# Kernel tuning notes

Hardware: AMD Instinct MI355X
Metric: run time of the kernel (lower is better)

The kernel has to match this reference:

```python
import jax, jax.numpy as jnp
import numpy as np

DIM = 1280
HEADS = 16
HEAD_DIM = DIM // HEADS  # 80
N_CHUNKS = 8
CHUNK = 1024
TOTAL = N_CHUNKS * CHUNK  # 8192 packed tokens


def rotate_half(x):
    x1, x2 = jnp.split(x, 2, axis=-1)
    return jnp.concatenate([-x2, x1], axis=-1)


def setup_inputs() -> dict:
    key = jax.random.key(0)
    k0, k1, k2 = jax.random.split(key, 3)
    hidden_states = jax.random.normal(k0, (TOTAL, DIM), dtype=jnp.float32)
    # 2D-rope style per-token angles, duplicated halves (standard vision RoPE layout)
    inv_freq = 1.0 / (10000.0 ** (jnp.arange(0, HEAD_DIM, 2, dtype=jnp.float32) / HEAD_DIM))
    pos = jnp.arange(TOTAL, dtype=jnp.float32)
    freqs = pos[:, None] * inv_freq[None, :]            # [T, HEAD_DIM//2]
    emb = jnp.concatenate([freqs, freqs], axis=-1)      # [T, HEAD_DIM]
    cos = jnp.cos(emb)
    sin = jnp.sin(emb)
    qkv_w = jax.random.normal(k1, (3 * DIM, DIM), dtype=jnp.float32) * 0.02
    qkv_b = jnp.zeros((3 * DIM,), dtype=jnp.float32)
    proj_w = jax.random.normal(k2, (DIM, DIM), dtype=jnp.float32) * 0.02
    proj_b = jnp.zeros((DIM,), dtype=jnp.float32)
    cu_seqlens = (jnp.arange(N_CHUNKS + 1, dtype=jnp.int32) * CHUNK)
    return {"hidden_states": hidden_states, "cos": cos, "sin": sin,
            "qkv_w": qkv_w, "qkv_b": qkv_b, "proj_w": proj_w, "proj_b": proj_b,
            "cu_seqlens": cu_seqlens}


def reference(hidden_states, cos, sin, qkv_w, qkv_b, proj_w, proj_b, cu_seqlens):
    # Equal-length chunks (cu_seqlens uniform): vectorize the Python chunk loop
    # as a leading batch axis n over chunks of length L.
    n = cu_seqlens.shape[0] - 1
    total, dim = hidden_states.shape
    L = total // n
    scaling = HEAD_DIM ** -0.5

    x = hidden_states.reshape(n, L, dim)
    qkv = x @ qkv_w.T + qkv_b                              # [n, L, 3*dim]
    qkv = qkv.reshape(n, L, 3, HEADS, HEAD_DIM)
    q, k, v = qkv[:, :, 0], qkv[:, :, 1], qkv[:, :, 2]     # [n, L, H, hd]

    # inline RoPE in fp32 (matches apply_rotary_pos_emb_vision)
    c = cos.reshape(n, L, 1, HEAD_DIM).astype(jnp.float32)
    s = sin.reshape(n, L, 1, HEAD_DIM).astype(jnp.float32)
    qf = q.astype(jnp.float32)
    kf = k.astype(jnp.float32)
    q = (qf * c + rotate_half(qf) * s).astype(q.dtype)
    k = (kf * c + rotate_half(kf) * s).astype(k.dtype)

    # naive per-chunk full attention: QK^T, fp32 softmax, PV
    scores = jnp.einsum('nlhd,nmhd->nhlm', q, k) * scaling  # [n, H, L, L]
    probs = jax.nn.softmax(scores.astype(jnp.float32), axis=-1).astype(q.dtype)
    out = jnp.einsum('nhlm,nmhd->nlhd', probs, v)           # [n, L, H, hd]
    out = out.reshape(n, L, dim)
    out = out @ proj_w.T + proj_b                           # [n, L, dim]
    return out.reshape(total, dim)
```

## Files before the change

kernel.cpp:

```cpp
#include <hip/hip_runtime.h>
#include <stdint.h>

#define DIM 1280
#define HEADS 16
#define HD 80
#define TOTAL 8192
#define CHUNK 1024
#define QKVN 3840

typedef __attribute__((ext_vector_type(8))) __bf16 bf16x8;
typedef __attribute__((ext_vector_type(4))) float floatx4;

typedef __attribute__((address_space(1))) const uint32_t gu32;
typedef __attribute__((address_space(3))) uint32_t lu32;

__device__ __forceinline__ void llds16(const void* g, void* l) {
  __builtin_amdgcn_global_load_lds((gu32*)g, (lu32*)l, 16, 0, 0);
}

__device__ __forceinline__ unsigned short f2b(float f) {
  union { __bf16 b; unsigned short u; } x; x.b = (__bf16)f; return x.u;
}
__device__ __forceinline__ float b2f(unsigned short u) {
  union { __bf16 b; unsigned short u; } x; x.u = u; return (float)x.b;
}
__device__ __forceinline__ float fexp2(float x) {
#if __has_builtin(__builtin_amdgcn_exp2f)
  return __builtin_amdgcn_exp2f(x);
#else
  return __expf(x * 0.6931471805599453f);
#endif
}

#define QSCALE (0.11180339887498949f * 1.44269504088896340f)

#define QROW 96
#define KT_SH (64 * 104)
#define VT_SH (80 * 72)

__global__ void cvt_bf16(const float* __restrict__ src, unsigned short* __restrict__ dst, int n4) {
  int i = blockIdx.x * 256 + threadIdx.x;
  if (i >= n4) return;
  float4 v = reinterpret_cast<const float4*>(src)[i];
  ushort4 o;
  o.x = f2b(v.x); o.y = f2b(v.y); o.z = f2b(v.z); o.w = f2b(v.w);
  reinterpret_cast<ushort4*>(dst)[i] = o;
}


__device__ __forceinline__ void stage_a64(const unsigned short* __restrict__ G,
                                          unsigned short* ls, int wv, int lane,
                                          int row0, int kk, int hi) {
#pragma unroll
  for (int t = 0; t < 2; ++t) {
    const int stripe = t * 8 + wv;
    const int rb = ((stripe >> 3) << 7) + ((stripe & 7) << 3) + hi;
    const int r = rb + (lane >> 3);
    const int ch = (lane & 7) ^ (r & 7);
    llds16(G + (size_t)(row0 + r) * DIM + kk + (ch << 3), ls + rb * 64);
  }
}

__device__ __forceinline__ void stage_b64(const unsigned short* __restrict__ G,
                                          unsigned short* ls, int wv, int lane,
                                          int row0, int kk, int hi) {
#pragma unroll
  for (int t = 0; t < 2; ++t) {
    const int stripe = t * 8 + wv;
    const int rb = ((stripe >> 2) << 6) + ((stripe & 3) << 3) + hi;
    const int r = rb + (lane >> 3);
    const int ch = (lane & 7) ^ (r & 7);
    llds16(G + (size_t)(row0 + r) * DIM + kk + (ch << 3), ls + rb * 64);
  }
}

__device__ __forceinline__ bf16x8 frg(const unsigned short* ls, int r, int cx) {
  return *reinterpret_cast<const bf16x8*>(ls + r * 64 + (cx << 3));
}

#define MFMA_BF16 __builtin_amdgcn_mfma_f32_16x16x32_bf16
#define LGKM0() asm volatile("s_waitcnt lgkmcnt(0)" ::: "memory")
#define BARR()  asm volatile("s_barrier" ::: "memory")

template<int MODE>
__launch_bounds__(512, 2)
__global__ void gemm8(const unsigned short* __restrict__ A,
                      const unsigned short* __restrict__ B,
                      const float* __restrict__ bias,
                      unsigned short* __restrict__ qo,
                      unsigned short* __restrict__ ko,
                      unsigned short* __restrict__ vo,
                      float* __restrict__ fo) {
  __shared__ __attribute__((aligned(16))) unsigned short lsA[2][256 * 64];
  __shared__ __attribute__((aligned(16))) unsigned short lsB[2][256 * 64];
  const int m0 = blockIdx.x * 256;
  const int n0 = blockIdx.y * 256;
  const int tid = threadIdx.x;
  const int wv = tid >> 6, lane = tid & 63;
  const int wr = wv >> 2, wc = wv & 3;
  const int q4 = lane >> 4, l15 = lane & 15;
  const int sx = l15 & 7;
  const int cx0 = q4 ^ sx;
  const int cx1 = (4 + q4) ^ sx;

  stage_a64(A, &lsA[0][0], wv, lane, m0, 0, 0);
  stage_b64(B, &lsB[0][0], wv, lane, n0, 0, 0);
  stage_b64(B, &lsB[0][0], wv, lane, n0, 0, 32);
  stage_a64(A, &lsA[0][0], wv, lane, m0, 0, 64);
  stage_b64(B, &lsB[1][0], wv, lane, n0, 64, 0);
  stage_a64(A, &lsA[1][0], wv, lane, m0, 64, 0);
  stage_b64(B, &lsB[1][0], wv, lane, n0, 64, 32);

  floatx4 acc[8][4];
#pragma unroll
  for (int i = 0; i < 8; ++i)
#pragma unroll
    for (int j = 0; j < 4; ++j)
      acc[i][j] = (floatx4){0.f, 0.f, 0.f, 0.f};

  asm volatile("s_waitcnt vmcnt(6)" ::: "memory");
  BARR();

  const int rA = wr * 128 + l15;
  const int rB = wc * 64 + l15;

  bf16x8 ArLo[4][2], ArHi[4][2], Blo[2][2], Bhi[2][2];

#pragma unroll 2
  for (int kt = 0; kt < 20; ++kt) {
    const unsigned short* la = &lsA[kt & 1][0];
    const unsigned short* lb = &lsB[kt & 1][0];
    unsigned short* aN = &lsA[(kt & 1) ^ 1][0];
    unsigned short* aC = &lsA[kt & 1][0];
    unsigned short* bC = &lsB[kt & 1][0];
    const bool st1 = (kt + 1 < 20);
    const bool st2 = (kt + 2 < 20);

    if (kt > 0) {
#pragma unroll
      for (int m = 0; m < 4; ++m)
#pragma unroll
        for (int n = 0; n < 2; ++n) {
          acc[m + 4][n] = MFMA_BF16(ArHi[m][0], Blo[n][0], acc[m + 4][n], 0, 0, 0);
          acc[m + 4][n] = MFMA_BF16(ArHi[m][1], Blo[n][1], acc[m + 4][n], 0, 0, 0);
        }
    }
#pragma unroll
    for (int m = 0; m < 4; ++m) {
      ArLo[m][0] = frg(la, rA + m * 16, cx0);
      ArLo[m][1] = frg(la, rA + m * 16, cx1);
    }
#pragma unroll
    for (int n = 0; n < 2; ++n) {
      Blo[n][0] = frg(lb, rB + n * 16, cx0);
      Blo[n][1] = frg(lb, rB + n * 16, cx1);
    }
    if (st1) stage_a64(A, aN, wv, lane, m0, (kt + 1) * 64, 64);
    LGKM0();
    BARR();

#pragma unroll
    for (int m = 0; m < 4; ++m)
#pragma unroll
      for (int n = 0; n < 2; ++n) {
        acc[m][n] = MFMA_BF16(ArLo[m][0], Blo[n][0], acc[m][n], 0, 0, 0);
        acc[m][n] = MFMA_BF16(ArLo[m][1], Blo[n][1], acc[m][n], 0, 0, 0);
      }
#pragma unroll
    for (int n = 0; n < 2; ++n) {
      Bhi[n][0] = frg(lb, rB + (n + 2) * 16, cx0);
      Bhi[n][1] = frg(lb, rB + (n + 2) * 16, cx1);
    }
    if (st2) stage_b64(B, bC, wv, lane, n0, (kt + 2) * 64, 0);
    LGKM0();
    BARR();

#pragma unroll
    for (int m = 0; m < 4; ++m)
#pragma unroll
      for (int n = 0; n < 2; ++n) {
        acc[m][n + 2] = MFMA_BF16(ArLo[m][0], Bhi[n][0], acc[m][n + 2], 0, 0, 0);
        acc[m][n + 2] = MFMA_BF16(ArLo[m][1], Bhi[n][1], acc[m][n + 2], 0, 0, 0);
      }
#pragma unroll
    for (int m = 0; m < 4; ++m) {
      ArHi[m][0] = frg(la, rA + (m + 4) * 16, cx0);
      ArHi[m][1] = frg(la, rA + (m + 4) * 16, cx1);
    }
    if (st2) stage_a64(A, aC, wv, lane, m0, (kt + 2) * 64, 0);
    LGKM0();
    BARR();

#pragma unroll
    for (int m = 0; m < 4; ++m)
#pragma unroll
      for (int n = 0; n < 2; ++n) {
        acc[m + 4][n + 2] = MFMA_BF16(ArHi[m][0], Bhi[n][0], acc[m + 4][n + 2], 0, 0, 0);
        acc[m + 4][n + 2] = MFMA_BF16(ArHi[m][1], Bhi[n][1], acc[m + 4][n + 2], 0, 0, 0);
      }
    if (st2) stage_b64(B, bC, wv, lane, n0, (kt + 2) * 64, 32);
    if (st2)      asm volatile("s_waitcnt vmcnt(6)" ::: "memory");
    else if (st1) asm volatile("s_waitcnt vmcnt(0)" ::: "memory");
    BARR();
  }

#pragma unroll
  for (int m = 0; m < 4; ++m)
#pragma unroll
    for (int n = 0; n < 2; ++n) {
      acc[m + 4][n] = MFMA_BF16(ArHi[m][0], Blo[n][0], acc[m + 4][n], 0, 0, 0);
      acc[m + 4][n] = MFMA_BF16(ArHi[m][1], Blo[n][1], acc[m + 4][n], 0, 0, 0);
    }

  if (MODE == 0) {
    if (blockIdx.y >= 10) {
      unsigned short* scr = (wv < 4) ? (&lsA[0][0] + wv * 8192)
                                     : (&lsB[0][0] + (wv - 4) * 8192);
      const int base_c = n0 - 2 * DIM + wc * 64;
#pragma unroll
      for (int n = 0; n < 4; ++n) {
        const int cloc = n * 16 + l15;
        const float bn = bias[2 * DIM + base_c + cloc];
        const int swz = (cloc & 7) << 4;
#pragma unroll
        for (int m = 0; m < 8; ++m) {
          const int rloc = m * 16 + q4 * 4;
          ushort4 w;
          w.x = f2b(acc[m][n][0] + bn);
          w.y = f2b(acc[m][n][1] + bn);
          w.z = f2b(acc[m][n][2] + bn);
          w.w = f2b(acc[m][n][3] + bn);
          *reinterpret_cast<ushort4*>(scr + cloc * 128 + (rloc ^ swz)) = w;
        }
      }
#pragma unroll
      for (int jtc = 0; jtc < 2; ++jtc) {
        const int rowg = m0 + wr * 128 + jtc * 64;
        const int chn = rowg >> 10, jtn = (rowg >> 6) & 15;
#pragma unroll
        for (int cb = 0; cb < 16; ++cb) {
          const int col = cb * 4 + q4;
          const int c = base_c + col;
          const int h = c / 80;
          const int d = c - h * 80;
          const int rloc = jtc * 64 + l15 * 4;
          const ushort4 w = *reinterpret_cast<const ushort4*>(
              scr + col * 128 + (rloc ^ ((col & 7) << 4)));
          *reinterpret_cast<ushort4*>(
              vo + (size_t)((chn * 16 + h) * 16 + jtn) * VT_SH + d * 72 + l15 * 4) = w;
        }
      }
      return;
    }
    unsigned short* os;
    int nloc = n0;
    if (blockIdx.y < 5) { os = qo; }
    else                { os = ko; nloc = n0 - DIM; }
#pragma unroll
    for (int n = 0; n < 4; ++n) {
      const int cg = wc * 64 + n * 16 + l15;
      const float bn = bias[n0 + cg];
#pragma unroll
      for (int m = 0; m < 8; ++m) {
#pragma unroll
        for (int r = 0; r < 4; ++r) {
          const int row = m0 + wr * 128 + m * 16 + q4 * 4 + r;
          os[(size_t)row * DIM + nloc + cg] = f2b(acc[m][n][r] + bn);
        }
      }
    }
    return;
  }
#pragma unroll
  for (int n = 0; n < 4; ++n) {
    const int cg = wc * 64 + n * 16 + l15;
    const float bn = bias[n0 + cg];
#pragma unroll
    for (int m = 0; m < 8; ++m) {
#pragma unroll
      for (int r = 0; r < 4; ++r) {
        const int row = m0 + wr * 128 + m * 16 + q4 * 4 + r;
        fo[(size_t)row * DIM + n0 + cg] = acc[m][n][r] + bn;
      }
    }
  }
}

__global__ void prep_qk(const unsigned short* __restrict__ qbuf,
                        const unsigned short* __restrict__ kbuf,
                        const float* __restrict__ cp, const float* __restrict__ sp,
                        unsigned short* __restrict__ qimg,
                        unsigned short* __restrict__ kimg) {
  const int m = blockIdx.x, tid = threadIdx.x;
  const int ch = m >> 10, rl = m & 1023;
  const int jt = rl >> 6, rr = rl & 63;

  if (tid < 160) {
    const int h = tid / 10, j = tid - h * 10;
    const int d0 = 4 * j;
    const float4 c4 = *reinterpret_cast<const float4*>(cp + (size_t)m * HD + d0);
    const float4 s4 = *reinterpret_cast<const float4*>(sp + (size_t)m * HD + d0);
    {
      const ushort4 lo = *reinterpret_cast<const ushort4*>(qbuf + (size_t)m * DIM + h * HD + d0);
      const ushort4 hi = *reinterpret_cast<const ushort4*>(qbuf + (size_t)m * DIM + h * HD + d0 + 40);
      ushort4 o1, o2;
      o1.x = f2b((b2f(lo.x) * c4.x - b2f(hi.x) * s4.x) * QSCALE);
      o1.y = f2b((b2f(lo.y) * c4.y - b2f(hi.y) * s4.y) * QSCALE);
      o1.z = f2b((b2f(lo.z) * c4.z - b2f(hi.z) * s4.z) * QSCALE);
      o1.w = f2b((b2f(lo.w) * c4.w - b2f(hi.w) * s4.w) * QSCALE);
      o2.x = f2b((b2f(hi.x) * c4.x + b2f(lo.x) * s4.x) * QSCALE);
      o2.y = f2b((b2f(hi.y) * c4.y + b2f(lo.y) * s4.y) * QSCALE);
      o2.z = f2b((b2f(hi.z) * c4.z + b2f(lo.z) * s4.z) * QSCALE);
      o2.w = f2b((b2f(hi.w) * c4.w + b2f(lo.w) * s4.w) * QSCALE);
      const size_t ob = ((size_t)(ch * 16 + h) * 1024 + rl) * QROW;
      *reinterpret_cast<ushort4*>(qimg + ob + d0) = o1;
      *reinterpret_cast<ushort4*>(qimg + ob + d0 + 40) = o2;
    }
    {
      const ushort4 lo = *reinterpret_cast<const ushort4*>(kbuf + (size_t)m * DIM + h * HD + d0);
      const ushort4 hi = *reinterpret_cast<const ushort4*>(kbuf + (size_t)m * DIM + h * HD + d0 + 40);
      ushort4 o1, o2;
      o1.x = f2b(b2f(lo.x) * c4.x - b2f(hi.x) * s4.x);
      o1.y = f2b(b2f(lo.y) * c4.y - b2f(hi.y) * s4.y);
      o1.z = f2b(b2f(lo.z) * c4.z - b2f(hi.z) * s4.z);
      o1.w = f2b(b2f(lo.w) * c4.w - b2f(hi.w) * s4.w);
      o2.x = f2b(b2f(hi.x) * c4.x + b2f(lo.x) * s4.x);
      o2.y = f2b(b2f(hi.y) * c4.y + b2f(lo.y) * s4.y);
      o2.z = f2b(b2f(hi.z) * c4.z + b2f(lo.z) * s4.z);
      o2.w = f2b(b2f(hi.w) * c4.w + b2f(lo.w) * s4.w);
      const size_t ob = ((size_t)((ch * 16 + h) * 16 + jt) * KT_SH) + rr * 104;
      *reinterpret_cast<ushort4*>(kimg + ob + d0) = o1;
      *reinterpret_cast<ushort4*>(kimg + ob + d0 + 40) = o2;
    }
  }
  if (tid < 64) {
    const int h = tid >> 2, qi = tid & 3;
    const size_t ob = ((size_t)(ch * 16 + h) * 1024 + rl) * QROW;
    *reinterpret_cast<ushort4*>(qimg + ob + 80 + 4 * qi) = (ushort4){0, 0, 0, 0};
  } else if (tid < 160) {
    const int t = tid - 64;
    const int h = t / 6, qi = t - h * 6;
    const size_t ob = ((size_t)((ch * 16 + h) * 16 + jt) * KT_SH) + rr * 104;
    *reinterpret_cast<ushort4*>(kimg + ob + 80 + 4 * qi) = (ushort4){0, 0, 0, 0};
  }
}

__launch_bounds__(256, 2)
__global__ void attn_k(const unsigned short* __restrict__ qimg,
                       const unsigned short* __restrict__ kimg,
                       const unsigned short* __restrict__ vimg,
                       unsigned short* __restrict__ ob) {
  __shared__ __attribute__((aligned(16))) unsigned short lsK[2][KT_SH];
  __shared__ __attribute__((aligned(16))) unsigned short lsV[2][VT_SH];
  __shared__ __attribute__((aligned(16))) unsigned short lsP[128 * 72];

  const int bx = blockIdx.x;
  const int qt = bx & 7, h = (bx >> 3) & 15, ch = bx >> 7;
  const int tid = threadIdx.x, wv = tid >> 6, lane = tid & 63;
  const int q4 = lane >> 4, l15 = lane & 15;
  const int qrow_loc = qt * 128 + wv * 32;

  bf16x8 aq[2][3];
  {
    const unsigned short* qb = qimg + ((size_t)(ch * 16 + h) * 1024 + qrow_loc) * QROW;
#pragma unroll
    for (int mt = 0; mt < 2; ++mt)
#pragma unroll
      for (int ks = 0; ks < 3; ++ks)
        aq[mt][ks] = *reinterpret_cast<const bf16x8*>(qb + (size_t)(mt * 16 + l15) * QROW + ks * 32 + q4 * 8);
  }

  floatx4 oacc[2][5];
  float lpart[2] = {0.f, 0.f};
#pragma unroll
  for (int mt = 0; mt < 2; ++mt)
#pragma unroll
    for (int t = 0; t < 5; ++t) oacc[mt][t] = (floatx4){0.f, 0.f, 0.f, 0.f};

  const char* kbase = (const char*)(kimg + (size_t)(ch * 16 + h) * 16 * KT_SH);
  const char* vbase = (const char*)(vimg + (size_t)(ch * 16 + h) * 16 * VT_SH);

  auto stage_kv = [&](int jt, char* lk, char* lv) {
    const char* kg = kbase + (size_t)jt * (KT_SH * 2);
#pragma unroll
    for (int r = 0; r < 4; ++r) {
      const int off = (r * 4 + wv) * 1024;
      if (off < KT_SH * 2)
        llds16(kg + off + lane * 16, lk + off);
    }
    const char* vg = vbase + (size_t)jt * (VT_SH * 2);
#pragma unroll
    for (int r = 0; r < 3; ++r) {
      const int off = (r * 4 + wv) * 1024;
      if (off < VT_SH * 2) {
        if (off + 1024 <= VT_SH * 2) llds16(vg + off + lane * 16, lv + off);
        else if (lane < 16)          llds16(vg + off + lane * 16, lv + off);
      }
    }
  };

  stage_kv(0, (char*)lsK[0], (char*)lsV[0]);

  for (int jt = 0; jt < 16; ++jt) {
    const int cur = jt & 1;
    __syncthreads();
    if (jt + 1 < 16)
      stage_kv(jt + 1, (char*)lsK[cur ^ 1], (char*)lsV[cur ^ 1]);

    const unsigned short* lk = lsK[cur];
    const unsigned short* lv = lsV[cur];

    floatx4 sfr[2][4];
    __builtin_amdgcn_s_setprio(1);
#pragma unroll
    for (int c = 0; c < 4; ++c) {
      const bf16x8 ak0 = *reinterpret_cast<const bf16x8*>(&lk[(c * 16 + l15) * 104 + 0  + q4 * 8]);
      const bf16x8 ak1 = *reinterpret_cast<const bf16x8*>(&lk[(c * 16 + l15) * 104 + 32 + q4 * 8]);
      const bf16x8 ak2 = *reinterpret_cast<const bf16x8*>(&lk[(c * 16 + l15) * 104 + 64 + q4 * 8]);
#pragma unroll
      for (int mt = 0; mt < 2; ++mt) {
        floatx4 s = (floatx4){0.f, 0.f, 0.f, 0.f};
        s = __builtin_amdgcn_mfma_f32_16x16x32_bf16(ak0, aq[mt][0], s, 0, 0, 0);
        s = __builtin_amdgcn_mfma_f32_16x16x32_bf16(ak1, aq[mt][1], s, 0, 0, 0);
        s = __builtin_amdgcn_mfma_f32_16x16x32_bf16(ak2, aq[mt][2], s, 0, 0, 0);
        sfr[mt][c] = s;
      }
    }
    __builtin_amdgcn_s_setprio(0);

#pragma unroll
    for (int mt = 0; mt < 2; ++mt)
#pragma unroll
      for (int c = 0; c < 4; ++c) {
        const float p0 = fexp2(sfr[mt][c][0]);
        const float p1 = fexp2(sfr[mt][c][1]);
        const float p2 = fexp2(sfr[mt][c][2]);
        const float p3 = fexp2(sfr[mt][c][3]);
        lpart[mt] += (p0 + p1) + (p2 + p3);
        ushort4 w;
        w.x = f2b(p0); w.y = f2b(p1); w.z = f2b(p2); w.w = f2b(p3);
        *reinterpret_cast<ushort4*>(&lsP[(wv * 32 + mt * 16 + l15) * 72 + c * 16 + q4 * 4]) = w;
      }

    __builtin_amdgcn_s_setprio(1);
#pragma unroll
    for (int ks = 0; ks < 2; ++ks) {
      const bf16x8 ap0 = *reinterpret_cast<const bf16x8*>(&lsP[(wv * 32 + 0  + l15) * 72 + ks * 32 + q4 * 8]);
      const bf16x8 ap1 = *reinterpret_cast<const bf16x8*>(&lsP[(wv * 32 + 16 + l15) * 72 + ks * 32 + q4 * 8]);
#pragma unroll
      for (int t = 0; t < 5; ++t) {
        const bf16x8 bv = *reinterpret_cast<const bf16x8*>(&lv[(t * 16 + l15) * 72 + ks * 32 + q4 * 8]);
        oacc[0][t] = __builtin_amdgcn_mfma_f32_16x16x32_bf16(ap0, bv, oacc[0][t], 0, 0, 0);
        oacc[1][t] = __builtin_amdgcn_mfma_f32_16x16x32_bf16(ap1, bv, oacc[1][t], 0, 0, 0);
      }
    }
    __builtin_amdgcn_s_setprio(0);
  }

#pragma unroll
  for (int mt = 0; mt < 2; ++mt) {
    lpart[mt] += __shfl_xor(lpart[mt], 16, 64);
    lpart[mt] += __shfl_xor(lpart[mt], 32, 64);
  }
  float inv[2];
  inv[0] = 1.0f / lpart[0];
  inv[1] = 1.0f / lpart[1];

  float invr[2][4];
#pragma unroll
  for (int mt = 0; mt < 2; ++mt)
#pragma unroll
    for (int r = 0; r < 4; ++r)
      invr[mt][r] = __shfl(inv[mt], q4 * 4 + r, 64);

#pragma unroll
  for (int mt = 0; mt < 2; ++mt)
#pragma unroll
    for (int t = 0; t < 5; ++t)
#pragma unroll
      for (int r = 0; r < 4; ++r) {
        const int gr = ch * CHUNK + qrow_loc + mt * 16 + q4 * 4 + r;
        const int gc = h * HD + t * 16 + l15;
        ob[(size_t)gr * DIM + gc] = f2b(oacc[mt][t][r] * invr[mt][r]);
      }
}

extern "C" void kernel_launch(void* const* d_in, const int* in_sizes, int n_in,
                              void* d_out, int out_size, void* d_ws, size_t ws_size,
                              hipStream_t stream) {
  (void)in_sizes; (void)n_in; (void)out_size; (void)ws_size;
  const float* hs    = (const float*)d_in[0];
  const float* cosp  = (const float*)d_in[1];
  const float* sinp  = (const float*)d_in[2];
  const float* qkvw  = (const float*)d_in[3];
  const float* qkvb  = (const float*)d_in[4];
  const float* projw = (const float*)d_in[5];
  const float* projb = (const float*)d_in[6];

  char* ws = (char*)d_ws;
  unsigned short* xb   = (unsigned short*)(ws + 0);
  unsigned short* wq   = (unsigned short*)(ws + 20971520);
  unsigned short* qbuf = (unsigned short*)(ws + 30801920);
  unsigned short* kbuf = (unsigned short*)(ws + 51773440);
  unsigned short* vimg = (unsigned short*)(ws + 72744960);
  unsigned short* wp   = (unsigned short*)(ws + 96337920);
  unsigned short* kimg = (unsigned short*)(ws + 99614720);
  unsigned short* qimg = (unsigned short*)(ws + 0);
  unsigned short* obuf = qbuf;

  cvt_bf16<<<TOTAL * DIM / 4 / 256, 256, 0, stream>>>(hs, xb, TOTAL * DIM / 4);
  cvt_bf16<<<QKVN * DIM / 4 / 256, 256, 0, stream>>>(qkvw, wq, QKVN * DIM / 4);
  cvt_bf16<<<DIM * DIM / 4 / 256, 256, 0, stream>>>(projw, wp, DIM * DIM / 4);

  gemm8<0><<<dim3(TOTAL / 256, QKVN / 256), 512, 0, stream>>>(
      xb, wq, qkvb, qbuf, kbuf, vimg, nullptr);

  prep_qk<<<TOTAL, 256, 0, stream>>>(qbuf, kbuf, cosp, sinp, qimg, kimg);

  attn_k<<<1024, 256, 0, stream>>>(qimg, kimg, vimg, obuf);

  gemm8<1><<<dim3(TOTAL / 256, DIM / 256), 512, 0, stream>>>(
      obuf, wp, projb, nullptr, nullptr, nullptr, (float*)d_out);
}
```

Baseline: 338.4 us.

## Fuse Q RoPE into attention load and remap block order for XCD locality

Q rotary embedding and scaling now happen inside the attention kernel when Q fragments are loaded, so the separate Q image write and read-back through global memory goes away and prep only handles K. Both GEMMs and the attention kernel remap block indices so that consecutive blocks on the same XCD share tiles, aiming for better L2 reuse. The cost is extra uncoalesced loads of Q, cos and sin per attention block, plus a changed workspace aliasing where the attention output now lands in the bf16 input buffer.

```diff
diff --git a/kernel.cpp b/kernel.cpp
--- a/kernel.cpp
+++ b/kernel.cpp
@@ -34,7 +34,6 @@
 
 #define QSCALE (0.11180339887498949f * 1.44269504088896340f)
 
-#define QROW 96
 #define KT_SH (64 * 104)
 #define VT_SH (80 * 72)
 
@@ -93,8 +92,13 @@
                       float* __restrict__ fo) {
   __shared__ __attribute__((aligned(16))) unsigned short lsA[2][256 * 64];
   __shared__ __attribute__((aligned(16))) unsigned short lsB[2][256 * 64];
-  const int m0 = blockIdx.x * 256;
-  const int n0 = blockIdx.y * 256;
+  const int nbk = gridDim.x * gridDim.y;
+  const int bid = blockIdx.y * gridDim.x + blockIdx.x;
+  const int nb = (bid & 7) * (nbk >> 3) + (bid >> 3);
+  const int bxm = nb % gridDim.x;
+  const int by = nb / gridDim.x;
+  const int m0 = bxm * 256;
+  const int n0 = by * 256;
   const int tid = threadIdx.x;
   const int wv = tid >> 6, lane = tid & 63;
   const int wr = wv >> 2, wc = wv & 3;
@@ -213,7 +217,7 @@
     }
 
   if (MODE == 0) {
-    if (blockIdx.y >= 10) {
+    if (by >= 10) {
       unsigned short* scr = (wv < 4) ? (&lsA[0][0] + wv * 8192)
                                      : (&lsB[0][0] + (wv - 4) * 8192);
       const int base_c = n0 - 2 * DIM + wc * 64;
@@ -254,8 +258,8 @@
     }
     unsigned short* os;
     int nloc = n0;
-    if (blockIdx.y < 5) { os = qo; }
-    else                { os = ko; nloc = n0 - DIM; }
+    if (by < 5) { os = qo; }
+    else        { os = ko; nloc = n0 - DIM; }
 #pragma unroll
     for (int n = 0; n < 4; ++n) {
       const int cg = wc * 64 + n * 16 + l15;
@@ -286,11 +290,9 @@
   }
 }
 
-__global__ void prep_qk(const unsigned short* __restrict__ qbuf,
-                        const unsigned short* __restrict__ kbuf,
-                        const float* __restrict__ cp, const float* __restrict__ sp,
-                        unsigned short* __restrict__ qimg,
-                        unsigned short* __restrict__ kimg) {
+__global__ void prep_k(const unsigned short* __restrict__ kbuf,
+                       const float* __restrict__ cp, const float* __restrict__ sp,
+                       unsigned short* __restrict__ kimg) {
   const int m = blockIdx.x, tid = threadIdx.x;
   const int ch = m >> 10, rl = m & 1023;
   const int jt = rl >> 6, rr = rl & 63;
@@ -300,45 +302,22 @@
     const int d0 = 4 * j;
     const float4 c4 = *reinterpret_cast<const float4*>(cp + (size_t)m * HD + d0);
     const float4 s4 = *reinterpret_cast<const float4*>(sp + (size_t)m * HD + d0);
-    {
-      const ushort4 lo = *reinterpret_cast<const ushort4*>(qbuf + (size_t)m * DIM + h * HD + d0);
-      const ushort4 hi = *reinterpret_cast<const ushort4*>(qbuf + (size_t)m * DIM + h * HD + d0 + 40);
-      ushort4 o1, o2;
-      o1.x = f2b((b2f(lo.x) * c4.x - b2f(hi.x) * s4.x) * QSCALE);
-      o1.y = f2b((b2f(lo.y) * c4.y - b2f(hi.y) * s4.y) * QSCALE);
-      o1.z = f2b((b2f(lo.z) * c4.z - b2f(hi.z) * s4.z) * QSCALE);
-      o1.w = f2b((b2f(lo.w) * c4.w - b2f(hi.w) * s4.w) * QSCALE);
-      o2.x = f2b((b2f(hi.x) * c4.x + b2f(lo.x) * s4.x) * QSCALE);
-      o2.y = f2b((b2f(hi.y) * c4.y + b2f(lo.y) * s4.y) * QSCALE);
-      o2.z = f2b((b2f(hi.z) * c4.z + b2f(lo.z) * s4.z) * QSCALE);
-      o2.w = f2b((b2f(hi.w) * c4.w + b2f(lo.w) * s4.w) * QSCALE);
-      const size_t ob = ((size_t)(ch * 16 + h) * 1024 + rl) * QROW;
-      *reinterpret_cast<ushort4*>(qimg + ob + d0) = o1;
-      *reinterpret_cast<ushort4*>(qimg + ob + d0 + 40) = o2;
-    }
-    {
-      const ushort4 lo = *reinterpret_cast<const ushort4*>(kbuf + (size_t)m * DIM + h * HD + d0);
-      const ushort4 hi = *reinterpret_cast<const ushort4*>(kbuf + (size_t)m * DIM + h * HD + d0 + 40);
-      ushort4 o1, o2;
-      o1.x = f2b(b2f(lo.x) * c4.x - b2f(hi.x) * s4.x);
-      o1.y = f2b(b2f(lo.y) * c4.y - b2f(hi.y) * s4.y);
-      o1.z = f2b(b2f(lo.z) * c4.z - b2f(hi.z) * s4.z);
-      o1.w = f2b(b2f(lo.w) * c4.w - b2f(hi.w) * s4.w);
-      o2.x = f2b(b2f(hi.x) * c4.x + b2f(lo.x) * s4.x);
-      o2.y = f2b(b2f(hi.y) * c4.y + b2f(lo.y) * s4.y);
-      o2.z = f2b(b2f(hi.z) * c4.z + b2f(lo.z) * s4.z);
-      o2.w = f2b(b2f(hi.w) * c4.w + b2f(lo.w) * s4.w);
-      const size_t ob = ((size_t)((ch * 16 + h) * 16 + jt) * KT_SH) + rr * 104;
-      *reinterpret_cast<ushort4*>(kimg + ob + d0) = o1;
-      *reinterpret_cast<ushort4*>(kimg + ob + d0 + 40) = o2;
-    }
-  }
-  if (tid < 64) {
-    const int h = tid >> 2, qi = tid & 3;
-    const size_t ob = ((size_t)(ch * 16 + h) * 1024 + rl) * QROW;
-    *reinterpret_cast<ushort4*>(qimg + ob + 80 + 4 * qi) = (ushort4){0, 0, 0, 0};
-  } else if (tid < 160) {
-    const int t = tid - 64;
+    const ushort4 lo = *reinterpret_cast<const ushort4*>(kbuf + (size_t)m * DIM + h * HD + d0);
+    const ushort4 hi = *reinterpret_cast<const ushort4*>(kbuf + (size_t)m * DIM + h * HD + d0 + 40);
+    ushort4 o1, o2;
+    o1.x = f2b(b2f(lo.x) * c4.x - b2f(hi.x) * s4.x);
+    o1.y = f2b(b2f(lo.y) * c4.y - b2f(hi.y) * s4.y);
+    o1.z = f2b(b2f(lo.z) * c4.z - b2f(hi.z) * s4.z);
+    o1.w = f2b(b2f(lo.w) * c4.w - b2f(hi.w) * s4.w);
+    o2.x = f2b(b2f(hi.x) * c4.x + b2f(lo.x) * s4.x);
+    o2.y = f2b(b2f(hi.y) * c4.y + b2f(lo.y) * s4.y);
+    o2.z = f2b(b2f(hi.z) * c4.z + b2f(lo.z) * s4.z);
+    o2.w = f2b(b2f(hi.w) * c4.w + b2f(lo.w) * s4.w);
+    const size_t ob = ((size_t)((ch * 16 + h) * 16 + jt) * KT_SH) + rr * 104;
+    *reinterpret_cast<ushort4*>(kimg + ob + d0) = o1;
+    *reinterpret_cast<ushort4*>(kimg + ob + d0 + 40) = o2;
+  } else {
+    const int t = tid - 160;
     const int h = t / 6, qi = t - h * 6;
     const size_t ob = ((size_t)((ch * 16 + h) * 16 + jt) * KT_SH) + rr * 104;
     *reinterpret_cast<ushort4*>(kimg + ob + 80 + 4 * qi) = (ushort4){0, 0, 0, 0};
@@ -346,28 +325,63 @@
 }
 
 __launch_bounds__(256, 2)
-__global__ void attn_k(const unsigned short* __restrict__ qimg,
+__global__ void attn_k(const unsigned short* __restrict__ qbuf,
                        const unsigned short* __restrict__ kimg,
                        const unsigned short* __restrict__ vimg,
+                       const float* __restrict__ cp, const float* __restrict__ sp,
                        unsigned short* __restrict__ ob) {
   __shared__ __attribute__((aligned(16))) unsigned short lsK[2][KT_SH];
   __shared__ __attribute__((aligned(16))) unsigned short lsV[2][VT_SH];
   __shared__ __attribute__((aligned(16))) unsigned short lsP[128 * 72];
 
-  const int bx = blockIdx.x;
-  const int qt = bx & 7, h = (bx >> 3) & 15, ch = bx >> 7;
+  const int i = blockIdx.x;
+  const int x = i & 7, t_ = i >> 3;
+  const int qt = t_ & 7;
+  const int g = (t_ >> 3) * 8 + x;
+  const int h = g & 15, ch = g >> 4;
   const int tid = threadIdx.x, wv = tid >> 6, lane = tid & 63;
   const int q4 = lane >> 4, l15 = lane & 15;
   const int qrow_loc = qt * 128 + wv * 32;
 
   bf16x8 aq[2][3];
-  {
-    const unsigned short* qb = qimg + ((size_t)(ch * 16 + h) * 1024 + qrow_loc) * QROW;
-#pragma unroll
-    for (int mt = 0; mt < 2; ++mt)
-#pragma unroll
-      for (int ks = 0; ks < 3; ++ks)
-        aq[mt][ks] = *reinterpret_cast<const bf16x8*>(qb + (size_t)(mt * 16 + l15) * QROW + ks * 32 + q4 * 8);
+#pragma unroll
+  for (int mt = 0; mt < 2; ++mt) {
+    const int m_row = ch * 1024 + qrow_loc + mt * 16 + l15;
+    const unsigned short* qr = qbuf + (size_t)m_row * DIM + h * HD;
+    const float* cr = cp + (size_t)m_row * HD;
+    const float* sr = sp + (size_t)m_row * HD;
+#pragma unroll
+    for (int ks = 0; ks < 3; ++ks) {
+      const int d0 = ks * 32 + q4 * 8;
+      union { ushort4 u4[2]; bf16x8 v; } out;
+      if (d0 < 80) {
+        const bool hi = (d0 >= 40);
+        const int pd = hi ? d0 - 40 : d0 + 40;
+        const float sg = hi ? 1.0f : -1.0f;
+        const ushort4 xa = *reinterpret_cast<const ushort4*>(qr + d0);
+        const ushort4 xc = *reinterpret_cast<const ushort4*>(qr + d0 + 4);
+        const ushort4 pa = *reinterpret_cast<const ushort4*>(qr + pd);
+        const ushort4 pc = *reinterpret_cast<const ushort4*>(qr + pd + 4);
+        const float4 c0 = *reinterpret_cast<const float4*>(cr + d0);
+        const float4 c1 = *reinterpret_cast<const float4*>(cr + d0 + 4);
+        const float4 s0 = *reinterpret_cast<const float4*>(sr + d0);
+        const float4 s1 = *reinterpret_cast<const float4*>(sr + d0 + 4);
+        ushort4 o0, o1;
+        o0.x = f2b((b2f(xa.x) * c0.x + sg * b2f(pa.x) * s0.x) * QSCALE);
+        o0.y = f2b((b2f(xa.y) * c0.y + sg * b2f(pa.y) * s0.y) * QSCALE);
+        o0.z = f2b((b2f(xa.z) * c0.z + sg * b2f(pa.z) * s0.z) * QSCALE);
+        o0.w = f2b((b2f(xa.w) * c0.w + sg * b2f(pa.w) * s0.w) * QSCALE);
+        o1.x = f2b((b2f(xc.x) * c1.x + sg * b2f(pc.x) * s1.x) * QSCALE);
+        o1.y = f2b((b2f(xc.y) * c1.y + sg * b2f(pc.y) * s1.y) * QSCALE);
+        o1.z = f2b((b2f(xc.z) * c1.z + sg * b2f(pc.z) * s1.z) * QSCALE);
+        o1.w = f2b((b2f(xc.w) * c1.w + sg * b2f(pc.w) * s1.w) * QSCALE);
+        out.u4[0] = o0; out.u4[1] = o1;
+      } else {
+        out.u4[0] = (ushort4){0, 0, 0, 0};
+        out.u4[1] = (ushort4){0, 0, 0, 0};
+      }
+      aq[mt][ks] = out.v;
+    }
   }
 
   floatx4 oacc[2][5];
@@ -505,8 +519,7 @@
   unsigned short* vimg = (unsigned short*)(ws + 72744960);
   unsigned short* wp   = (unsigned short*)(ws + 96337920);
   unsigned short* kimg = (unsigned short*)(ws + 99614720);
-  unsigned short* qimg = (unsigned short*)(ws + 0);
-  unsigned short* obuf = qbuf;
+  unsigned short* obuf = xb;
 
   cvt_bf16<<<TOTAL * DIM / 4 / 256, 256, 0, stream>>>(hs, xb, TOTAL * DIM / 4);
   cvt_bf16<<<QKVN * DIM / 4 / 256, 256, 0, stream>>>(qkvw, wq, QKVN * DIM / 4);
@@ -515,9 +528,9 @@
   gemm8<0><<<dim3(TOTAL / 256, QKVN / 256), 512, 0, stream>>>(
       xb, wq, qkvb, qbuf, kbuf, vimg, nullptr);
 
-  prep_qk<<<TOTAL, 256, 0, stream>>>(qbuf, kbuf, cosp, sinp, qimg, kimg);
-
-  attn_k<<<1024, 256, 0, stream>>>(qimg, kimg, vimg, obuf);
+  prep_k<<<TOTAL, 256, 0, stream>>>(kbuf, cosp, sinp, kimg);
+
+  attn_k<<<1024, 256, 0, stream>>>(qbuf, kimg, vimg, cosp, sinp, obuf);
 
   gemm8<1><<<dim3(TOTAL / 256, DIM / 256), 512, 0, stream>>>(
       obuf, wp, projb, nullptr, nullptr, nullptr, (float*)d_out);
```

Measured after the change: 353.3 us. +4.4%, slower.
